# Optimization experiments

Hardware: AMD Instinct MI355X
Metric: run time of the kernel (lower is better)

The kernel has to match this reference:

```python
import jax, jax.numpy as jnp
import numpy as np

INPT, HID, NNODE, K, B = 64, 128, 10000, 16, 8

def setup_inputs() -> dict:
    key = jax.random.key(0)
    ks = jax.random.split(key, 12)
    def lin(k, fan_in, fan_out):
        # orthogonal-ish init stand-in; exact init values are irrelevant for the reference math
        return jax.random.normal(k, (fan_in, fan_out), jnp.float32) / np.sqrt(fan_in)
    return {
        "state": jax.random.normal(ks[0], (B, NNODE, INPT), jnp.float32),
        "internal": jax.random.normal(ks[1], (B, NNODE, INPT), jnp.float32),
        "state_neigh": jax.random.randint(ks[2], (NNODE, K), 0, NNODE),
        "internal_neigh": jax.random.randint(ks[3], (NNODE, K), 0, NNODE),
        "W1": lin(ks[4], INPT, HID), "b1": jnp.zeros((HID,), jnp.float32),
        "W2": lin(ks[5], HID, HID), "b2": jnp.zeros((HID,), jnp.float32),
        "Wu1": lin(ks[6], 2 * HID, HID), "bu1": jnp.zeros((HID,), jnp.float32),
        "Wu2": lin(ks[7], 2 * HID, HID), "bu2": jnp.zeros((HID,), jnp.float32),
    }

def _aggregate(se, ie, s_idx, i_idx):
    # se, ie: [B, N, H]; idx: [N, K] -> gather neighbors and sum over K
    g_s = jnp.take(se, s_idx, axis=1).sum(axis=2)   # [B, N, H]
    g_i = jnp.take(ie, i_idx, axis=1).sum(axis=2)   # [B, N, H]
    return g_s + g_i

def _update(aggr, h, W, b):
    x = jnp.concatenate((aggr, h), axis=-1)          # [B, N, 2H]
    return jax.nn.relu(x @ W + b)

def reference(state, internal, state_neigh, internal_neigh,
              W1, b1, W2, b2, Wu1, bu1, Wu2, bu2):
    # layer-1 embeddings
    state_embed = jax.nn.relu(state @ W1 + b1)       # [B, N, H]
    internal_embed = jax.nn.relu(internal @ W1 + b1)
    aggr1 = _aggregate(state_embed, internal_embed, state_neigh, internal_neigh)
    hu1 = _update(aggr1, internal_embed, Wu1, bu1)   # [B, N, H]
    # layer-2 embeddings
    se2 = jax.nn.relu(state_embed @ W2 + b2)
    ie2 = jax.nn.relu(hu1 @ W2 + b2)
    aggr2 = _aggregate(se2, ie2, state_neigh, internal_neigh)
    hu2 = _update(aggr2, ie2, Wu2, bu2)              # [B, N, H]
    return hu1, hu2
```

## Files before the change

kernel.cpp:

```cpp
#include <hip/hip_runtime.h>

#define HID 128
#define NNODE 10000
#define KN 16
#define ROWS 80000
#define UROWS 32

typedef __attribute__((ext_vector_type(8))) short short8;
typedef __attribute__((ext_vector_type(4))) float f32x4;

__device__ __forceinline__ unsigned short f2b(float f) {
    unsigned u = __float_as_uint(f);
    u += 0x7FFFu + ((u >> 16) & 1u);
    return (unsigned short)(u >> 16);
}
__device__ __forceinline__ float b2f(unsigned short h) {
    return __uint_as_float(((unsigned)h) << 16);
}

__global__ __launch_bounds__(256) void wconv_all(
    const float* __restrict__ W1, const float* __restrict__ W2,
    const float* __restrict__ Wu1, const float* __restrict__ Wu2,
    unsigned short* __restrict__ W1t, unsigned short* __restrict__ W2t,
    unsigned short* __restrict__ Wu1t, unsigned short* __restrict__ Wu2t) {
    int idx = blockIdx.x * 256 + threadIdx.x;
    const float* W; unsigned short* Wt; int K; int off;
    if (idx < 8192)       { W = W1;  Wt = W1t;  K = 64;  off = idx; }
    else if (idx < 24576) { W = W2;  Wt = W2t;  K = 128; off = idx - 8192; }
    else if (idx < 57344) { W = Wu1; Wt = Wu1t; K = 256; off = idx - 24576; }
    else                  { W = Wu2; Wt = Wu2t; K = 256; off = idx - 57344; }
    int n = off & 127, k = off >> 7;
    Wt[n * K + k] = f2b(W[off]);
}

template<int K, bool AF32>
__global__ __launch_bounds__(256) void embed_mfma(
    const void* __restrict__ A0, const void* __restrict__ A1,
    const unsigned short* __restrict__ Wt, const float* __restrict__ bias,
    unsigned short* __restrict__ Y0, unsigned short* __restrict__ Y1) {
    int g = blockIdx.x;
    const void* Ain = A0; unsigned short* Yb = Y0;
    if (g >= 1250) { Ain = A1; Yb = Y1; g -= 1250; }

    const int wave = threadIdx.x >> 6, lane = threadIdx.x & 63;
    const int lrow = lane & 15, lk = lane >> 4;
    const int m0 = g * 64 + wave * 16;
    const int arow = m0 + lrow;

    short8 a[K / 32];
    if constexpr (AF32) {
        const float* A = (const float*)Ain;
#pragma unroll
        for (int kt = 0; kt < K / 32; ++kt) {
            const float* p = A + (size_t)arow * K + kt * 32 + lk * 8;
            f32x4 f0 = *(const f32x4*)p;
            f32x4 f1 = *(const f32x4*)(p + 4);
            short8 v;
#pragma unroll
            for (int e = 0; e < 4; ++e) { v[e] = (short)f2b(f0[e]); v[4 + e] = (short)f2b(f1[e]); }
            a[kt] = v;
        }
    } else {
        const unsigned short* A = (const unsigned short*)Ain;
#pragma unroll
        for (int kt = 0; kt < K / 32; ++kt)
            a[kt] = *(const short8*)(A + (size_t)arow * K + kt * 32 + lk * 8);
    }

#pragma unroll
    for (int nt = 0; nt < 8; ++nt) {
        f32x4 acc = {0.f, 0.f, 0.f, 0.f};
#pragma unroll
        for (int kt = 0; kt < K / 32; ++kt) {
            short8 b = *(const short8*)(Wt + (nt * 16 + lrow) * K + kt * 32 + lk * 8);
            acc = __builtin_amdgcn_mfma_f32_16x16x32_bf16(a[kt], b, acc, 0, 0, 0);
        }
        const int ocol = nt * 16 + lrow;
        const float bv = bias[ocol];
#pragma unroll
        for (int j = 0; j < 4; ++j) {
            const int orow = m0 + lk * 4 + j;
            float v = acc[j] + bv;
            v = v > 0.f ? v : 0.f;
            Yb[(size_t)orow * HID + ocol] = f2b(v);
        }
    }
}

__global__ __launch_bounds__(512) void update_mfma(
    const unsigned short* __restrict__ SE, const unsigned short* __restrict__ IE,
    const int* __restrict__ sidx, const int* __restrict__ iidx,
    const unsigned short* __restrict__ Wut, const float* __restrict__ bu,
    float* __restrict__ Yf, unsigned short* __restrict__ Yb, int writeb) {
    __shared__ __align__(16) unsigned short At[UROWS * 256];
    __shared__ int sh_idx[32][UROWS];
    char* Ab = (char*)At;
    const int t = threadIdx.x;
    const int b = blockIdx.x & 7;
    const int n0 = (blockIdx.x >> 3) * UROWS;
    const size_t base = (size_t)b * NNODE * HID;

#pragma unroll
    for (int h = 0; h < 2; ++h) {
        const int e = t + h * 512;
        const int r = e >> 5, k = e & 31;
        const int nr = n0 + r < NNODE ? n0 + r : NNODE - 1;
        sh_idx[k][r] = (k < KN) ? sidx[nr * KN + k] : iidx[nr * KN + (k - KN)];
    }
    __syncthreads();

    {
        const int r = t >> 4;
        const int p = t & 15;
        const int col0 = p * 8;
        const int nr = n0 + r < NNODE ? n0 + r : NNODE - 1;

        float acc[8];
#pragma unroll
        for (int e = 0; e < 8; ++e) acc[e] = 0.f;

#pragma unroll
        for (int k = 0; k < KN; ++k) {
            const int ns = sh_idx[k][r];
            short8 v = *(const short8*)(SE + base + (size_t)ns * HID + col0);
#pragma unroll
            for (int e = 0; e < 8; ++e) acc[e] += b2f((unsigned short)v[e]);
        }
#pragma unroll
        for (int k = 0; k < KN; ++k) {
            const int ni = sh_idx[KN + k][r];
            short8 v = *(const short8*)(IE + base + (size_t)ni * HID + col0);
#pragma unroll
            for (int e = 0; e < 8; ++e) acc[e] += b2f((unsigned short)v[e]);
        }
        short8 v;
#pragma unroll
        for (int e = 0; e < 8; ++e) v[e] = (short)f2b(acc[e]);
        *(short8*)(Ab + r * 512 + ((col0 * 2) ^ ((r & 7) << 4))) = v;
        short8 hv = *(const short8*)(IE + base + (size_t)nr * HID + col0);
        *(short8*)(Ab + r * 512 + ((256 + col0 * 2) ^ ((r & 7) << 4))) = hv;
    }
    __syncthreads();

    const int wave = t >> 6, lane = t & 63;
    const int lrow = lane & 15, lk = lane >> 4;
    const int rowg = wave & 1, colg = wave >> 1;
    const int row = rowg * 16 + lrow;

    short8 a[8];
#pragma unroll
    for (int kt = 0; kt < 8; ++kt)
        a[kt] = *(const short8*)(Ab + row * 512 + ((kt * 64 + lk * 16) ^ ((row & 7) << 4)));

#pragma unroll
    for (int nt2 = 0; nt2 < 2; ++nt2) {
        const int nt = colg * 2 + nt2;
        f32x4 acc = {0.f, 0.f, 0.f, 0.f};
#pragma unroll
        for (int kt = 0; kt < 8; ++kt) {
            short8 bb = *(const short8*)(Wut + (nt * 16 + lrow) * 256 + kt * 32 + lk * 8);
            acc = __builtin_amdgcn_mfma_f32_16x16x32_bf16(a[kt], bb, acc, 0, 0, 0);
        }
        const int ocol = nt * 16 + lrow;
        const float bv = bu[ocol];
#pragma unroll
        for (int j = 0; j < 4; ++j) {
            const int rr = rowg * 16 + lk * 4 + j;
            const int n_o = n0 + rr;
            if (n_o < NNODE) {
                const size_t orow = (size_t)b * NNODE + n_o;
                float vv = acc[j] + bv;
                vv = vv > 0.f ? vv : 0.f;
                Yf[orow * HID + ocol] = vv;
                if (writeb) Yb[orow * HID + ocol] = f2b(vv);
            }
        }
    }
}

extern "C" void kernel_launch(void* const* d_in, const int* in_sizes, int n_in,
                              void* d_out, int out_size, void* d_ws, size_t ws_size,
                              hipStream_t stream) {
    const float* state    = (const float*)d_in[0];
    const float* internal = (const float*)d_in[1];
    const int*   sidx     = (const int*)d_in[2];
    const int*   iidx     = (const int*)d_in[3];
    const float* W1  = (const float*)d_in[4];
    const float* b1  = (const float*)d_in[5];
    const float* W2  = (const float*)d_in[6];
    const float* b2  = (const float*)d_in[7];
    const float* Wu1 = (const float*)d_in[8];
    const float* bu1 = (const float*)d_in[9];
    const float* Wu2 = (const float*)d_in[10];
    const float* bu2 = (const float*)d_in[11];

    float* hu1 = (float*)d_out;
    float* hu2 = hu1 + (size_t)ROWS * HID;

    unsigned short* W1t  = (unsigned short*)d_ws;
    unsigned short* W2t  = W1t  + 64 * 128;
    unsigned short* Wu1t = W2t  + 128 * 128;
    unsigned short* Wu2t = Wu1t + 256 * 128;
    unsigned short* bufA = Wu2t + 256 * 128;
    unsigned short* bufB = bufA + (size_t)ROWS * HID;
    unsigned short* bufC = bufB + (size_t)ROWS * HID;

    dim3 b256(256), b512(512);

    wconv_all<<<352, b256, 0, stream>>>(W1, W2, Wu1, Wu2, W1t, W2t, Wu1t, Wu2t);

    embed_mfma<64, true><<<2500, b256, 0, stream>>>(state, internal, W1t, b1, bufA, bufB);

    update_mfma<<<8 * 313, b512, 0, stream>>>(bufA, bufB, sidx, iidx, Wu1t, bu1, hu1, bufC, 1);

    embed_mfma<128, false><<<1250, b256, 0, stream>>>(bufA, nullptr, W2t, b2, bufB, nullptr);
    embed_mfma<128, false><<<1250, b256, 0, stream>>>(bufC, nullptr, W2t, b2, bufA, nullptr);

    update_mfma<<<8 * 313, b512, 0, stream>>>(bufB, bufA, sidx, iidx, Wu2t, bu2, hu2, nullptr, 0);
}
```

Before: 253.0 us.

## Batch neighbor gathers for memory-level parallelism and merge layer-2 embed launches

```diff
diff --git a/kernel.cpp b/kernel.cpp
--- a/kernel.cpp
+++ b/kernel.cpp
@@ -8,14 +8,14 @@
 
 typedef __attribute__((ext_vector_type(8))) short short8;
 typedef __attribute__((ext_vector_type(4))) float f32x4;
+typedef __attribute__((ext_vector_type(2))) float f32x2;
+typedef __attribute__((ext_vector_type(4))) int i32x4;
+typedef __attribute__((ext_vector_type(4))) unsigned int u32x4;
 
 __device__ __forceinline__ unsigned short f2b(float f) {
     unsigned u = __float_as_uint(f);
     u += 0x7FFFu + ((u >> 16) & 1u);
     return (unsigned short)(u >> 16);
-}
-__device__ __forceinline__ float b2f(unsigned short h) {
-    return __uint_as_float(((unsigned)h) << 16);
 }
 
 __global__ __launch_bounds__(256) void wconv_all(
@@ -87,13 +87,13 @@
     }
 }
 
-__global__ __launch_bounds__(512) void update_mfma(
+__global__ __launch_bounds__(512, 4) void update_mfma(
     const unsigned short* __restrict__ SE, const unsigned short* __restrict__ IE,
     const int* __restrict__ sidx, const int* __restrict__ iidx,
     const unsigned short* __restrict__ Wut, const float* __restrict__ bu,
     float* __restrict__ Yf, unsigned short* __restrict__ Yb, int writeb) {
     __shared__ __align__(16) unsigned short At[UROWS * 256];
-    __shared__ int sh_idx[32][UROWS];
+    __shared__ __align__(16) int sh_idx[UROWS][36];
     char* Ab = (char*)At;
     const int t = threadIdx.x;
     const int b = blockIdx.x & 7;
@@ -104,8 +104,8 @@
     for (int h = 0; h < 2; ++h) {
         const int e = t + h * 512;
         const int r = e >> 5, k = e & 31;
-        const int nr = n0 + r < NNODE ? n0 + r : NNODE - 1;
-        sh_idx[k][r] = (k < KN) ? sidx[nr * KN + k] : iidx[nr * KN + (k - KN)];
+        const int nr = min(n0 + r, NNODE - 1);
+        sh_idx[r][k] = (k < KN) ? sidx[nr * KN + k] : iidx[nr * KN + (k - KN)];
     }
     __syncthreads();
 
@@ -113,31 +113,58 @@
         const int r = t >> 4;
         const int p = t & 15;
         const int col0 = p * 8;
-        const int nr = n0 + r < NNODE ? n0 + r : NNODE - 1;
-
-        float acc[8];
-#pragma unroll
-        for (int e = 0; e < 8; ++e) acc[e] = 0.f;
-
-#pragma unroll
-        for (int k = 0; k < KN; ++k) {
-            const int ns = sh_idx[k][r];
-            short8 v = *(const short8*)(SE + base + (size_t)ns * HID + col0);
-#pragma unroll
-            for (int e = 0; e < 8; ++e) acc[e] += b2f((unsigned short)v[e]);
-        }
-#pragma unroll
-        for (int k = 0; k < KN; ++k) {
-            const int ni = sh_idx[KN + k][r];
-            short8 v = *(const short8*)(IE + base + (size_t)ni * HID + col0);
-#pragma unroll
-            for (int e = 0; e < 8; ++e) acc[e] += b2f((unsigned short)v[e]);
-        }
-        short8 v;
-#pragma unroll
-        for (int e = 0; e < 8; ++e) v[e] = (short)f2b(acc[e]);
-        *(short8*)(Ab + r * 512 + ((col0 * 2) ^ ((r & 7) << 4))) = v;
+        const int nr = min(n0 + r, NNODE - 1);
+        const unsigned short* Sb = SE + base + col0;
+        const unsigned short* Ib = IE + base + col0;
+
         short8 hv = *(const short8*)(IE + base + (size_t)nr * HID + col0);
+
+        f32x2 acc[4];
+#pragma unroll
+        for (int j = 0; j < 4; ++j) acc[j] = (f32x2){0.f, 0.f};
+
+        u32x4 vals[16];
+        i32x4 iv[4];
+
+#pragma unroll
+        for (int q = 0; q < 4; ++q) iv[q] = *(const i32x4*)&sh_idx[r][q * 4];
+#pragma unroll
+        for (int q = 0; q < 4; ++q)
+#pragma unroll
+            for (int j = 0; j < 4; ++j)
+                vals[q * 4 + j] = *(const u32x4*)(Sb + (size_t)iv[q][j] * HID);
+#pragma unroll
+        for (int k = 0; k < 16; ++k)
+#pragma unroll
+            for (int j = 0; j < 4; ++j) {
+                const unsigned u = vals[k][j];
+                f32x2 pr = {__uint_as_float(u << 16), __uint_as_float(u & 0xffff0000u)};
+                acc[j] += pr;
+            }
+
+#pragma unroll
+        for (int q = 0; q < 4; ++q) iv[q] = *(const i32x4*)&sh_idx[r][16 + q * 4];
+#pragma unroll
+        for (int q = 0; q < 4; ++q)
+#pragma unroll
+            for (int j = 0; j < 4; ++j)
+                vals[q * 4 + j] = *(const u32x4*)(Ib + (size_t)iv[q][j] * HID);
+#pragma unroll
+        for (int k = 0; k < 16; ++k)
+#pragma unroll
+            for (int j = 0; j < 4; ++j) {
+                const unsigned u = vals[k][j];
+                f32x2 pr = {__uint_as_float(u << 16), __uint_as_float(u & 0xffff0000u)};
+                acc[j] += pr;
+            }
+
+        short8 ov;
+#pragma unroll
+        for (int j = 0; j < 4; ++j) {
+            ov[2 * j]     = (short)f2b(acc[j].x);
+            ov[2 * j + 1] = (short)f2b(acc[j].y);
+        }
+        *(short8*)(Ab + r * 512 + ((col0 * 2) ^ ((r & 7) << 4))) = ov;
         *(short8*)(Ab + r * 512 + ((256 + col0 * 2) ^ ((r & 7) << 4))) = hv;
     }
     __syncthreads();
@@ -204,6 +231,10 @@
     unsigned short* bufA = Wu2t + 256 * 128;
     unsigned short* bufB = bufA + (size_t)ROWS * HID;
     unsigned short* bufC = bufB + (size_t)ROWS * HID;
+    unsigned short* bufD = bufC + (size_t)ROWS * HID;
+
+    const size_t need4 = (size_t)(90112) * 2 + 4 * (size_t)ROWS * HID * 2;
+    const bool big = ws_size >= need4;
 
     dim3 b256(256), b512(512);
 
@@ -213,8 +244,12 @@
 
     update_mfma<<<8 * 313, b512, 0, stream>>>(bufA, bufB, sidx, iidx, Wu1t, bu1, hu1, bufC, 1);
 
-    embed_mfma<128, false><<<1250, b256, 0, stream>>>(bufA, nullptr, W2t, b2, bufB, nullptr);
-    embed_mfma<128, false><<<1250, b256, 0, stream>>>(bufC, nullptr, W2t, b2, bufA, nullptr);
-
-    update_mfma<<<8 * 313, b512, 0, stream>>>(bufB, bufA, sidx, iidx, Wu2t, bu2, hu2, nullptr, 0);
-}
+    if (big) {
+        embed_mfma<128, false><<<2500, b256, 0, stream>>>(bufA, bufC, W2t, b2, bufB, bufD);
+        update_mfma<<<8 * 313, b512, 0, stream>>>(bufB, bufD, sidx, iidx, Wu2t, bu2, hu2, nullptr, 0);
+    } else {
+        embed_mfma<128, false><<<1250, b256, 0, stream>>>(bufA, nullptr, W2t, b2, bufB, nullptr);
+        embed_mfma<128, false><<<1250, b256, 0, stream>>>(bufC, nullptr, W2t, b2, bufA, nullptr);
+        update_mfma<<<8 * 313, b512, 0, stream>>>(bufB, bufA, sidx, iidx, Wu2t, bu2, hu2, nullptr, 0);
+    }
+}
```

New measurement: 244.9 us. 3.2% less time.

## Split gather-aggregate from update GEMM and merge layer-2 embed launches

Applied to the files above, without the earlier changes.

```diff
diff --git a/kernel.cpp b/kernel.cpp
--- a/kernel.cpp
+++ b/kernel.cpp
@@ -4,18 +4,17 @@
 #define NNODE 10000
 #define KN 16
 #define ROWS 80000
-#define UROWS 32
+#define NCHUNK 157
 
 typedef __attribute__((ext_vector_type(8))) short short8;
 typedef __attribute__((ext_vector_type(4))) float f32x4;
+typedef __attribute__((ext_vector_type(2))) float f32x2;
+typedef __attribute__((ext_vector_type(4))) unsigned int u32x4;
 
 __device__ __forceinline__ unsigned short f2b(float f) {
     unsigned u = __float_as_uint(f);
     u += 0x7FFFu + ((u >> 16) & 1u);
     return (unsigned short)(u >> 16);
-}
-__device__ __forceinline__ float b2f(unsigned short h) {
-    return __uint_as_float(((unsigned)h) << 16);
 }
 
 __global__ __launch_bounds__(256) void wconv_all(
@@ -87,92 +86,106 @@
     }
 }
 
-__global__ __launch_bounds__(512) void update_mfma(
+__global__ __launch_bounds__(512) void aggr_kernel(
     const unsigned short* __restrict__ SE, const unsigned short* __restrict__ IE,
     const int* __restrict__ sidx, const int* __restrict__ iidx,
+    unsigned short* __restrict__ G) {
+    __shared__ int sh_idx[64][33];
+    const int t = threadIdx.x;
+    const int b = blockIdx.x & 7;
+    const int hc = blockIdx.x >> 3;
+    const int h = hc >= NCHUNK ? 1 : 0;
+    const int c = hc - h * NCHUNK;
+    const int n0 = c * 64;
+
+#pragma unroll
+    for (int q = 0; q < 4; ++q) {
+        const int e = t + q * 512;
+        const int r = e >> 5, k = e & 31;
+        int nr = n0 + r; if (nr > NNODE - 1) nr = NNODE - 1;
+        sh_idx[r][k] = (k < KN) ? sidx[nr * KN + k] : iidx[nr * KN + (k - KN)];
+    }
+    __syncthreads();
+
+    const int r = t >> 3, p = t & 7;
+    const int col0 = h * 64 + p * 8;
+    const int n = n0 + r;
+    const size_t base = (size_t)b * NNODE * HID + col0;
+
+    f32x2 acc[4];
+#pragma unroll
+    for (int w = 0; w < 4; ++w) acc[w] = (f32x2){0.f, 0.f};
+
+#pragma unroll
+    for (int q = 0; q < 4; ++q) {
+        const unsigned short* P = (q < 2) ? SE : IE;
+        u32x4 vals[8];
+#pragma unroll
+        for (int j = 0; j < 8; ++j)
+            vals[j] = *(const u32x4*)(P + base + (size_t)sh_idx[r][q * 8 + j] * HID);
+#pragma unroll
+        for (int j = 0; j < 8; ++j)
+#pragma unroll
+            for (int w = 0; w < 4; ++w) {
+                const unsigned u = vals[j][w];
+                acc[w] += (f32x2){__uint_as_float(u << 16), __uint_as_float(u & 0xffff0000u)};
+            }
+    }
+
+    if (n < NNODE) {
+        short8 ov;
+#pragma unroll
+        for (int w = 0; w < 4; ++w) {
+            ov[2 * w]     = (short)f2b(acc[w].x);
+            ov[2 * w + 1] = (short)f2b(acc[w].y);
+        }
+        *(short8*)(G + ((size_t)b * NNODE + n) * HID + col0) = ov;
+    }
+}
+
+__global__ __launch_bounds__(512) void update_gemm(
+    const unsigned short* __restrict__ G, const unsigned short* __restrict__ H,
     const unsigned short* __restrict__ Wut, const float* __restrict__ bu,
     float* __restrict__ Yf, unsigned short* __restrict__ Yb, int writeb) {
-    __shared__ __align__(16) unsigned short At[UROWS * 256];
-    __shared__ int sh_idx[32][UROWS];
-    char* Ab = (char*)At;
-    const int t = threadIdx.x;
-    const int b = blockIdx.x & 7;
-    const int n0 = (blockIdx.x >> 3) * UROWS;
-    const size_t base = (size_t)b * NNODE * HID;
-
-#pragma unroll
-    for (int h = 0; h < 2; ++h) {
-        const int e = t + h * 512;
-        const int r = e >> 5, k = e & 31;
-        const int nr = n0 + r < NNODE ? n0 + r : NNODE - 1;
-        sh_idx[k][r] = (k < KN) ? sidx[nr * KN + k] : iidx[nr * KN + (k - KN)];
-    }
-    __syncthreads();
-
-    {
-        const int r = t >> 4;
-        const int p = t & 15;
-        const int col0 = p * 8;
-        const int nr = n0 + r < NNODE ? n0 + r : NNODE - 1;
-
-        float acc[8];
-#pragma unroll
-        for (int e = 0; e < 8; ++e) acc[e] = 0.f;
-
-#pragma unroll
-        for (int k = 0; k < KN; ++k) {
-            const int ns = sh_idx[k][r];
-            short8 v = *(const short8*)(SE + base + (size_t)ns * HID + col0);
-#pragma unroll
-            for (int e = 0; e < 8; ++e) acc[e] += b2f((unsigned short)v[e]);
-        }
-#pragma unroll
-        for (int k = 0; k < KN; ++k) {
-            const int ni = sh_idx[KN + k][r];
-            short8 v = *(const short8*)(IE + base + (size_t)ni * HID + col0);
-#pragma unroll
-            for (int e = 0; e < 8; ++e) acc[e] += b2f((unsigned short)v[e]);
-        }
-        short8 v;
-#pragma unroll
-        for (int e = 0; e < 8; ++e) v[e] = (short)f2b(acc[e]);
-        *(short8*)(Ab + r * 512 + ((col0 * 2) ^ ((r & 7) << 4))) = v;
-        short8 hv = *(const short8*)(IE + base + (size_t)nr * HID + col0);
-        *(short8*)(Ab + r * 512 + ((256 + col0 * 2) ^ ((r & 7) << 4))) = hv;
-    }
-    __syncthreads();
-
-    const int wave = t >> 6, lane = t & 63;
+    const int t = threadIdx.x, wave = t >> 6, lane = t & 63;
     const int lrow = lane & 15, lk = lane >> 4;
-    const int rowg = wave & 1, colg = wave >> 1;
-    const int row = rowg * 16 + lrow;
-
-    short8 a[8];
-#pragma unroll
-    for (int kt = 0; kt < 8; ++kt)
-        a[kt] = *(const short8*)(Ab + row * 512 + ((kt * 64 + lk * 16) ^ ((row & 7) << 4)));
+    const int rs = wave & 1, colg = wave >> 1;
+    const int m0 = blockIdx.x * 64 + rs * 32;
+    const int row0 = m0 + lrow, row1 = m0 + 16 + lrow;
+
+    short8 a0[8], a1[8];
+#pragma unroll
+    for (int kt = 0; kt < 4; ++kt) {
+        a0[kt]     = *(const short8*)(G + (size_t)row0 * HID + kt * 32 + lk * 8);
+        a1[kt]     = *(const short8*)(G + (size_t)row1 * HID + kt * 32 + lk * 8);
+        a0[4 + kt] = *(const short8*)(H + (size_t)row0 * HID + kt * 32 + lk * 8);
+        a1[4 + kt] = *(const short8*)(H + (size_t)row1 * HID + kt * 32 + lk * 8);
+    }
 
 #pragma unroll
     for (int nt2 = 0; nt2 < 2; ++nt2) {
         const int nt = colg * 2 + nt2;
-        f32x4 acc = {0.f, 0.f, 0.f, 0.f};
+        f32x4 acc0 = {0.f, 0.f, 0.f, 0.f};
+        f32x4 acc1 = {0.f, 0.f, 0.f, 0.f};
 #pragma unroll
         for (int kt = 0; kt < 8; ++kt) {
             short8 bb = *(const short8*)(Wut + (nt * 16 + lrow) * 256 + kt * 32 + lk * 8);
-            acc = __builtin_amdgcn_mfma_f32_16x16x32_bf16(a[kt], bb, acc, 0, 0, 0);
+            acc0 = __builtin_amdgcn_mfma_f32_16x16x32_bf16(a0[kt], bb, acc0, 0, 0, 0);
+            acc1 = __builtin_amdgcn_mfma_f32_16x16x32_bf16(a1[kt], bb, acc1, 0, 0, 0);
         }
         const int ocol = nt * 16 + lrow;
         const float bv = bu[ocol];
 #pragma unroll
         for (int j = 0; j < 4; ++j) {
-            const int rr = rowg * 16 + lk * 4 + j;
-            const int n_o = n0 + rr;
-            if (n_o < NNODE) {
-                const size_t orow = (size_t)b * NNODE + n_o;
-                float vv = acc[j] + bv;
-                vv = vv > 0.f ? vv : 0.f;
-                Yf[orow * HID + ocol] = vv;
-                if (writeb) Yb[orow * HID + ocol] = f2b(vv);
+            const size_t r0 = (size_t)m0 + lk * 4 + j;
+            const size_t r1 = r0 + 16;
+            float v0 = acc0[j] + bv; v0 = v0 > 0.f ? v0 : 0.f;
+            float v1 = acc1[j] + bv; v1 = v1 > 0.f ? v1 : 0.f;
+            Yf[r0 * HID + ocol] = v0;
+            Yf[r1 * HID + ocol] = v1;
+            if (writeb) {
+                Yb[r0 * HID + ocol] = f2b(v0);
+                Yb[r1 * HID + ocol] = f2b(v1);
             }
         }
     }
@@ -204,17 +217,31 @@
     unsigned short* bufA = Wu2t + 256 * 128;
     unsigned short* bufB = bufA + (size_t)ROWS * HID;
     unsigned short* bufC = bufB + (size_t)ROWS * HID;
+    unsigned short* bufD = bufC + (size_t)ROWS * HID;
+
+    const size_t need4 = (size_t)90112 * 2 + 4 * (size_t)ROWS * HID * 2;
+    const bool big = ws_size >= need4;
 
     dim3 b256(256), b512(512);
+    const int AGRID = 8 * 2 * NCHUNK;
 
     wconv_all<<<352, b256, 0, stream>>>(W1, W2, Wu1, Wu2, W1t, W2t, Wu1t, Wu2t);
 
     embed_mfma<64, true><<<2500, b256, 0, stream>>>(state, internal, W1t, b1, bufA, bufB);
 
-    update_mfma<<<8 * 313, b512, 0, stream>>>(bufA, bufB, sidx, iidx, Wu1t, bu1, hu1, bufC, 1);
-
-    embed_mfma<128, false><<<1250, b256, 0, stream>>>(bufA, nullptr, W2t, b2, bufB, nullptr);
-    embed_mfma<128, false><<<1250, b256, 0, stream>>>(bufC, nullptr, W2t, b2, bufA, nullptr);
-
-    update_mfma<<<8 * 313, b512, 0, stream>>>(bufB, bufA, sidx, iidx, Wu2t, bu2, hu2, nullptr, 0);
-}
+    if (big) {
+        aggr_kernel<<<AGRID, b512, 0, stream>>>(bufA, bufB, sidx, iidx, bufD);
+        update_gemm<<<1250, b512, 0, stream>>>(bufD, bufB, Wu1t, bu1, hu1, bufC, 1);
+        embed_mfma<128, false><<<2500, b256, 0, stream>>>(bufA, bufC, W2t, b2, bufB, bufD);
+        aggr_kernel<<<AGRID, b512, 0, stream>>>(bufB, bufD, sidx, iidx, bufA);
+        update_gemm<<<1250, b512, 0, stream>>>(bufA, bufD, Wu2t, bu2, hu2, nullptr, 0);
+    } else {
+        unsigned short* Ghu2 = (unsigned short*)hu2;
+        aggr_kernel<<<AGRID, b512, 0, stream>>>(bufA, bufB, sidx, iidx, Ghu2);
+        update_gemm<<<1250, b512, 0, stream>>>(Ghu2, bufB, Wu1t, bu1, hu1, bufC, 1);
+        embed_mfma<128, false><<<1250, b256, 0, stream>>>(bufA, nullptr, W2t, b2, bufB, nullptr);
+        embed_mfma<128, false><<<1250, b256, 0, stream>>>(bufC, nullptr, W2t, b2, bufA, nullptr);
+        aggr_kernel<<<AGRID, b512, 0, stream>>>(bufB, bufA, sidx, iidx, bufC);
+        update_gemm<<<1250, b512, 0, stream>>>(bufC, bufA, Wu2t, bu2, hu2, nullptr, 0);
+    }
+}
```

Measured after the change: 250.2 us. No clear change (-1.1%).
